# Kernel tuning notes

Hardware: AMD Instinct MI355X
Metric: run time of the kernel (lower is better)

## Reference

```python
import jax, jax.numpy as jnp
import numpy as np

# conf[1:] and loss_div_wd[1:] tables from the original module (31 entries each)
CONF = np.float32([0.9991138577461243, 0.8724386692047119, 0.8048540353775024, 0.7398145198822021, 0.6715637445449829, 0.5973713397979736, 0.5154045820236206, 0.42423248291015625, 0.3226756751537323, 0.20976418256759644, 0.08473344892263412, -0.05296758562326431, -0.2036692053079605, -0.3674810528755188, -0.5443023443222046, -0.7338425517082214, -0.9356498718261719, -1.149145483970642, -1.3736592531204224, -1.6084641218185425, -1.8528070449829102, -2.1059343814849854, -2.367111921310425, -2.6356399059295654, -2.910861015319824, -3.1921679973602295, -3.479003667831421, -3.770861864089966, -4.067285060882568, -4.367861747741699, -4.67222261428833])
LOSS_DIV_WD = np.float32([-0.7357585932962737, -0.7292385198866751, -0.7197861042909649, -0.7060825529685993, -0.6862159572880272, -0.6574145455480526, -0.6156599675844636, -0.5551266577364037, -0.46736905653740307, -0.34014329294487, -0.15569892914556094, 0.11169756647530316, 0.4993531412919867, 1.0613531942004133, 1.8761075276533326, 3.0572900212223724, 4.769698321281568, 7.252246278161051, 10.851297017399714, 16.06898724880869, 23.63328498268829, 34.599555050301056, 50.497802769609315, 73.54613907594951, 106.96024960367691, 155.40204460004963, 225.63008495214464, 327.4425312511471, 475.0441754009414, 689.0282819387658, 999.249744])

_LOG = np.log(LOSS_DIV_WD + np.float32(0.750256)).astype(np.float32)
LOG_STEP = np.float32((_LOG[-1] - _LOG[0]) / 2.0)   # step * (N-1) / 2
LOG_OFFSET = np.float32(_LOG[0] + LOG_STEP)
NTAB = CONF.shape[0]  # 31

B, NCLS, NSAMPLES = 32768, 1000, 1000000
SMOOTH_INS = 0.9
SMOOTH_CLS = 0.9
WD_INS = 1.0
WD_CLS = 1.0


def optimal_conf(loss, wd):
    # 1D linear interp emulating F.grid_sample(..., padding_mode='border', align_corners=True)
    l = loss / wd
    ln = (jnp.log(l + 0.750256) - LOG_OFFSET) / LOG_STEP
    ln = jnp.where(jnp.isnan(ln), -1.0, ln)          # NaN (log of negative) -> left border
    ix = jnp.clip((ln + 1.0) * 0.5 * (NTAB - 1), 0.0, NTAB - 1)
    i0 = jnp.floor(ix)
    frac = ix - i0
    i0 = i0.astype(jnp.int32)
    i1 = jnp.minimum(i0 + 1, NTAB - 1)
    tab = jnp.asarray(CONF)
    r = tab[i0] * (1.0 - frac) + tab[i1] * frac
    return jnp.exp(r)


def smoothed(values, idx, memory, smoothing, nseg):
    # EMA smoothing per bin: bincount-with-weights -> per-bin mean -> alpha = smoothing**count
    binned = jax.ops.segment_sum(values, idx, num_segments=nseg)
    cnt = jax.ops.segment_sum(jnp.ones_like(values), idx, num_segments=nseg)
    nnz = cnt > 0
    means = jnp.where(nnz, binned / jnp.maximum(cnt, 1.0), 0.0)
    alpha = smoothing ** cnt
    new_mem = jnp.where(nnz, alpha * memory + (1.0 - alpha) * means, memory)
    return new_mem[idx]


def setup_inputs() -> dict:
    key = jax.random.key(0)
    k1, k2, k3 = jax.random.split(key, 3)
    preds = jax.random.normal(k1, (B, NCLS), dtype=jnp.float32)
    labels = jax.random.randint(k2, (B,), 0, NCLS, dtype=jnp.int32)
    indices = jax.random.randint(k3, (B,), 0, NSAMPLES, dtype=jnp.int32)
    memory_ins = jnp.zeros((NSAMPLES,), dtype=jnp.float32)
    memory_cls = jnp.zeros((NCLS,), dtype=jnp.float32)
    return {"preds": preds, "memory_ins": memory_ins, "memory_cls": memory_cls,
            "labels": labels, "indices": indices}


def reference(preds, memory_ins, memory_cls, labels, indices):
    # per-sample cross entropy (reduction='none')
    logp = jax.nn.log_softmax(preds, axis=-1)
    loss_batch = -jnp.take_along_axis(logp, labels[:, None].astype(jnp.int32), axis=-1)[:, 0]
    lb = jax.lax.stop_gradient(loss_batch)  # loss_batch.detach()
    # instance branch (expectation = Constant(0) -> threshold 0)
    sl_ins = smoothed(lb, indices, memory_ins, SMOOTH_INS, NSAMPLES)
    conf_ins = optimal_conf(sl_ins, WD_INS)
    # class branch
    sl_cls = smoothed(lb, labels, memory_cls, SMOOTH_CLS, NCLS)
    conf_cls = optimal_conf(sl_cls, WD_CLS)
    conf = jax.lax.stop_gradient(conf_ins * conf_cls)
    return (loss_batch * conf).mean()
```

## Files before the change

kernel.cpp:

```cpp
#include <hip/hip_runtime.h>
#include <math.h>

#define B_N 32768
#define NCLS 1000
#define NSAMP 1000000
#define NTAB 31

__constant__ float c_conf[NTAB] = {
    0.9991138577461243f, 0.8724386692047119f, 0.8048540353775024f, 0.7398145198822021f,
    0.6715637445449829f, 0.5973713397979736f, 0.5154045820236206f, 0.42423248291015625f,
    0.3226756751537323f, 0.20976418256759644f, 0.08473344892263412f, -0.05296758562326431f,
    -0.2036692053079605f, -0.3674810528755188f, -0.5443023443222046f, -0.7338425517082214f,
    -0.9356498718261719f, -1.149145483970642f, -1.3736592531204224f, -1.6084641218185425f,
    -1.8528070449829102f, -2.1059343814849854f, -2.367111921310425f, -2.6356399059295654f,
    -2.910861015319824f, -3.1921679973602295f, -3.479003667831421f, -3.770861864089966f,
    -4.067285060882568f, -4.367861747741699f, -4.67222261428833f};

#define LOG_OFFSET 1.3369849f
#define INV_LOG_STEP 0.17950834f
#define LN_SMOOTH -0.10536052f

__device__ __forceinline__ float optimal_conf(float l) {
    float ln = (logf(l + 0.750256f) - LOG_OFFSET) * INV_LOG_STEP;
    if (ln != ln) ln = -1.0f;
    float ix = fminf(fmaxf((ln + 1.0f) * 0.5f * (NTAB - 1), 0.0f), (float)(NTAB - 1));
    float i0f = floorf(ix);
    float frac = ix - i0f;
    int i0 = (int)i0f;
    int i1 = min(i0 + 1, NTAB - 1);
    float r = c_conf[i0] * (1.0f - frac) + c_conf[i1] * frac;
    return expf(r);
}

__global__ __launch_bounds__(256) void ce_loss_kernel(
    const float* __restrict__ preds, const int* __restrict__ labels,
    const int* __restrict__ indices, float* __restrict__ loss,
    float* __restrict__ ins_sum, float* __restrict__ ins_cnt,
    float* __restrict__ cls_sum, float* __restrict__ cls_cnt)
{
    const int row = blockIdx.x;
    const int t = threadIdx.x;
    const float4* p = (const float4*)(preds + (size_t)row * NCLS);

    float4 v = make_float4(-INFINITY, -INFINITY, -INFINITY, -INFINITY);
    if (t < NCLS / 4) v = p[t];

    float m = fmaxf(fmaxf(v.x, v.y), fmaxf(v.z, v.w));
    #pragma unroll
    for (int off = 32; off > 0; off >>= 1) m = fmaxf(m, __shfl_down(m, off, 64));
    __shared__ float sm[4];
    __shared__ float bcast;
    const int wave = t >> 6, lane = t & 63;
    if (lane == 0) sm[wave] = m;
    __syncthreads();
    if (t == 0) bcast = fmaxf(fmaxf(sm[0], sm[1]), fmaxf(sm[2], sm[3]));
    __syncthreads();
    const float M = bcast;

    float s = 0.0f;
    if (t < NCLS / 4)
        s = expf(v.x - M) + expf(v.y - M) + expf(v.z - M) + expf(v.w - M);
    #pragma unroll
    for (int off = 32; off > 0; off >>= 1) s += __shfl_down(s, off, 64);
    __syncthreads();
    if (lane == 0) sm[wave] = s;
    __syncthreads();

    if (t == 0) {
        const float S = sm[0] + sm[1] + sm[2] + sm[3];
        const int lab = labels[row];
        const float l = logf(S) + M - preds[(size_t)row * NCLS + lab];
        loss[row] = l;
        const int idx = indices[row];
        atomicAdd(&ins_sum[idx], l);
        atomicAdd(&ins_cnt[idx], 1.0f);
        atomicAdd(&cls_sum[lab], l);
        atomicAdd(&cls_cnt[lab], 1.0f);
    }
}

__global__ __launch_bounds__(256) void conf_reduce_kernel(
    const float* __restrict__ loss, const int* __restrict__ labels,
    const int* __restrict__ indices,
    const float* __restrict__ mem_ins, const float* __restrict__ mem_cls,
    const float* __restrict__ ins_sum, const float* __restrict__ ins_cnt,
    const float* __restrict__ cls_sum, const float* __restrict__ cls_cnt,
    float* __restrict__ out)
{
    const int i = blockIdx.x * 256 + threadIdx.x;
    float val = 0.0f;
    if (i < B_N) {
        const float l = loss[i];
        const int idx = indices[i];
        const int lab = labels[i];

        const float ci = ins_cnt[idx];
        const float mean_i = ins_sum[idx] / ci;
        const float ai = expf(ci * LN_SMOOTH);
        const float sl_i = ai * mem_ins[idx] + (1.0f - ai) * mean_i;

        const float cc = cls_cnt[lab];
        const float mean_c = cls_sum[lab] / cc;
        const float ac = expf(cc * LN_SMOOTH);
        const float sl_c = ac * mem_cls[lab] + (1.0f - ac) * mean_c;

        const float conf = optimal_conf(sl_i) * optimal_conf(sl_c);
        val = l * conf * (1.0f / (float)B_N);
    }
    #pragma unroll
    for (int off = 32; off > 0; off >>= 1) val += __shfl_down(val, off, 64);
    __shared__ float sm[4];
    const int wave = threadIdx.x >> 6, lane = threadIdx.x & 63;
    if (lane == 0) sm[wave] = val;
    __syncthreads();
    if (threadIdx.x == 0) atomicAdd(out, sm[0] + sm[1] + sm[2] + sm[3]);
}

extern "C" void kernel_launch(void* const* d_in, const int* in_sizes, int n_in,
                              void* d_out, int out_size, void* d_ws, size_t ws_size,
                              hipStream_t stream) {
    const float* preds   = (const float*)d_in[0];
    const float* mem_ins = (const float*)d_in[1];
    const float* mem_cls = (const float*)d_in[2];
    const int*   labels  = (const int*)d_in[3];
    const int*   indices = (const int*)d_in[4];
    float* out = (float*)d_out;

    float* loss    = (float*)d_ws;
    float* ins_sum = loss + B_N;
    float* ins_cnt = ins_sum + NSAMP;
    float* cls_sum = ins_cnt + NSAMP;
    float* cls_cnt = cls_sum + NCLS;

    hipMemsetAsync(ins_sum, 0, (size_t)(2 * NSAMP + 2 * NCLS) * sizeof(float), stream);
    hipMemsetAsync(out, 0, sizeof(float), stream);

    ce_loss_kernel<<<B_N, 256, 0, stream>>>(preds, labels, indices, loss,
                                            ins_sum, ins_cnt, cls_sum, cls_cnt);
    conf_reduce_kernel<<<(B_N + 255) / 256, 256, 0, stream>>>(
        loss, labels, indices, mem_ins, mem_cls,
        ins_sum, ins_cnt, cls_sum, cls_cnt, out);
}
```

Measured before the change: 200.2 us.

## Assign one wavefront per row in cross-entropy kernel, dropping block syncs

The cross-entropy kernel now maps each row to a single 64-lane wavefront instead of a 256-thread block. Each lane loads up to four float4s, and the max and sum reductions are done with wave shuffles only, with no shared memory or __syncthreads. The label logit is picked out of registers and reduced together with the sum, which avoids a dependent global reload. Grid size drops by four and per-block sync overhead goes away, at the cost of more registers per thread.

```diff
diff --git a/kernel.cpp b/kernel.cpp
--- a/kernel.cpp
+++ b/kernel.cpp
@@ -5,6 +5,7 @@
 #define NCLS 1000
 #define NSAMP 1000000
 #define NTAB 31
+#define NF4 250
 
 __constant__ float c_conf[NTAB] = {
     0.9991138577461243f, 0.8724386692047119f, 0.8048540353775024f, 0.7398145198822021f,
@@ -32,44 +33,57 @@
     return expf(r);
 }
 
+__device__ __forceinline__ float pick(float4 v, int c) {
+    return c == 0 ? v.x : (c == 1 ? v.y : (c == 2 ? v.z : v.w));
+}
+
 __global__ __launch_bounds__(256) void ce_loss_kernel(
     const float* __restrict__ preds, const int* __restrict__ labels,
     const int* __restrict__ indices, float* __restrict__ loss,
     float* __restrict__ ins_sum, float* __restrict__ ins_cnt,
     float* __restrict__ cls_sum, float* __restrict__ cls_cnt)
 {
-    const int row = blockIdx.x;
-    const int t = threadIdx.x;
+    const int wave = threadIdx.x >> 6;
+    const int lane = threadIdx.x & 63;
+    const int row = (blockIdx.x << 2) + wave;
+
     const float4* p = (const float4*)(preds + (size_t)row * NCLS);
+    const int lab = labels[row];
+    const int labj = lab >> 2, labc = lab & 3;
 
-    float4 v = make_float4(-INFINITY, -INFINITY, -INFINITY, -INFINITY);
-    if (t < NCLS / 4) v = p[t];
+    const float NEG = -INFINITY;
+    float4 v0 = p[lane];
+    float4 v1 = p[lane + 64];
+    float4 v2 = p[lane + 128];
+    float4 v3 = make_float4(NEG, NEG, NEG, NEG);
+    if (lane + 192 < NF4) v3 = p[lane + 192];
 
-    float m = fmaxf(fmaxf(v.x, v.y), fmaxf(v.z, v.w));
+    float pl = 0.0f;
+    if (labj == lane)            pl = pick(v0, labc);
+    else if (labj == lane + 64)  pl = pick(v1, labc);
+    else if (labj == lane + 128) pl = pick(v2, labc);
+    else if (labj == lane + 192) pl = pick(v3, labc);
+
+    float m = fmaxf(fmaxf(fmaxf(v0.x, v0.y), fmaxf(v0.z, v0.w)),
+                    fmaxf(fmaxf(v1.x, v1.y), fmaxf(v1.z, v1.w)));
+    m = fmaxf(m, fmaxf(fmaxf(v2.x, v2.y), fmaxf(v2.z, v2.w)));
+    m = fmaxf(m, fmaxf(fmaxf(v3.x, v3.y), fmaxf(v3.z, v3.w)));
     #pragma unroll
     for (int off = 32; off > 0; off >>= 1) m = fmaxf(m, __shfl_down(m, off, 64));
-    __shared__ float sm[4];
-    __shared__ float bcast;
-    const int wave = t >> 6, lane = t & 63;
-    if (lane == 0) sm[wave] = m;
-    __syncthreads();
-    if (t == 0) bcast = fmaxf(fmaxf(sm[0], sm[1]), fmaxf(sm[2], sm[3]));
-    __syncthreads();
-    const float M = bcast;
+    m = __shfl(m, 0, 64);
 
-    float s = 0.0f;
-    if (t < NCLS / 4)
-        s = expf(v.x - M) + expf(v.y - M) + expf(v.z - M) + expf(v.w - M);
+    float s = expf(v0.x - m) + expf(v0.y - m) + expf(v0.z - m) + expf(v0.w - m)
+            + expf(v1.x - m) + expf(v1.y - m) + expf(v1.z - m) + expf(v1.w - m)
+            + expf(v2.x - m) + expf(v2.y - m) + expf(v2.z - m) + expf(v2.w - m)
+            + expf(v3.x - m) + expf(v3.y - m) + expf(v3.z - m) + expf(v3.w - m);
     #pragma unroll
-    for (int off = 32; off > 0; off >>= 1) s += __shfl_down(s, off, 64);
-    __syncthreads();
-    if (lane == 0) sm[wave] = s;
-    __syncthreads();
+    for (int off = 32; off > 0; off >>= 1) {
+        s  += __shfl_down(s, off, 64);
+        pl += __shfl_down(pl, off, 64);
+    }
 
-    if (t == 0) {
-        const float S = sm[0] + sm[1] + sm[2] + sm[3];
-        const int lab = labels[row];
-        const float l = logf(S) + M - preds[(size_t)row * NCLS + lab];
+    if (lane == 0) {
+        const float l = logf(s) + m - pl;
         loss[row] = l;
         const int idx = indices[row];
         atomicAdd(&ins_sum[idx], l);
@@ -135,8 +149,8 @@
     hipMemsetAsync(ins_sum, 0, (size_t)(2 * NSAMP + 2 * NCLS) * sizeof(float), stream);
     hipMemsetAsync(out, 0, sizeof(float), stream);
 
-    ce_loss_kernel<<<B_N, 256, 0, stream>>>(preds, labels, indices, loss,
-                                            ins_sum, ins_cnt, cls_sum, cls_cnt);
+    ce_loss_kernel<<<B_N / 4, 256, 0, stream>>>(preds, labels, indices, loss,
+                                                ins_sum, ins_cnt, cls_sum, cls_cnt);
     conf_reduce_kernel<<<(B_N + 255) / 256, 256, 0, stream>>>(
         loss, labels, indices, mem_ins, mem_cls,
         ins_sum, ins_cnt, cls_sum, cls_cnt, out);
```

Result: no change. 201.9 us (+0.8%).
